# Kernel tuning notes

Measured on AMD Instinct MI355X. Metric: run time of the kernel, lower is better.

The kernel has to match this reference:

```python
import jax, jax.numpy as jnp
import numpy as np

HEADS = 4
AGENT = 49  # 7x7 agent tokens
LN_EPS = 1e-5


def setup_inputs() -> dict:
    key = jax.random.key(0)
    ks = jax.random.split(key, 3)
    B, C, H, W = 2, 128, 56, 56
    x = jax.random.normal(ks[0], (B, C, H, W), jnp.float32)
    # 1x1 convs == per-pixel linear maps; store as [out_ch, in_ch]
    w_qkv = jax.random.normal(ks[1], (3 * C, C), jnp.float32) * (C ** -0.5)
    w_proj = jax.random.normal(ks[2], (C, C), jnp.float32) * (C ** -0.5)
    b_proj = jnp.zeros((C,), jnp.float32)
    ln_g = jnp.ones((C,), jnp.float32)
    ln_b = jnp.zeros((C,), jnp.float32)
    return {"x": x, "w_qkv": w_qkv, "w_proj": w_proj, "b_proj": b_proj,
            "ln_g": ln_g, "ln_b": ln_b}


def reference(x, w_qkv, w_proj, b_proj, ln_g, ln_b):
    B, C, H, W = x.shape
    heads = HEADS
    hd = C // heads
    N = H * W
    scale = hd ** -0.5
    a = int(AGENT ** 0.5)  # 7; H,W divisible by a -> exact adaptive avg pool

    # 1x1-conv QKV: [B,3C,H,W] -> [B,3,heads,hd,N] -> q,k,v [B,h,N,hd]
    qkv = jnp.einsum('oc,bchw->bohw', w_qkv, x).reshape(B, 3, heads, hd, N)
    q = jnp.transpose(qkv[:, 0], (0, 1, 3, 2))
    k = jnp.transpose(qkv[:, 1], (0, 1, 3, 2))
    v = jnp.transpose(qkv[:, 2], (0, 1, 3, 2))

    # agent tokens: adaptive avg pool to (a,a) == uniform block mean
    agent = x.reshape(B, C, a, H // a, a, W // a).mean(axis=(3, 5))  # [B,C,a,a]
    agent = agent.reshape(B, heads, hd, AGENT)
    agent = jnp.transpose(agent, (0, 1, 3, 2))  # [B,h,A,hd]

    # stage 1: compress q through agent tokens
    q_to_agent = jax.nn.softmax(
        jnp.einsum('bhnd,bhad->bhna', q * scale, agent), axis=-1)  # [B,h,N,A]
    q_compressed = jnp.einsum('bhna,bhad->bhnd', q_to_agent, agent)  # [B,h,N,hd]

    # stage 2: full N x N attention with compressed queries
    attn = jax.nn.softmax(
        jnp.einsum('bhnd,bhmd->bhnm', q_compressed * scale, k), axis=-1)
    out = jnp.einsum('bhnm,bhmd->bhnd', attn, v)  # [B,h,N,hd]

    # merge heads -> [B,N,C], 1x1-conv proj, LayerNorm over C
    out = jnp.transpose(out, (0, 2, 1, 3)).reshape(B, N, C)
    out = jnp.einsum('bnc,oc->bno', out, w_proj) + b_proj
    mu = out.mean(-1, keepdims=True)
    var = out.var(-1, keepdims=True)
    out = (out - mu) / jnp.sqrt(var + LN_EPS) * ln_g + ln_b
    return jnp.transpose(out.reshape(B, H, W, C), (0, 3, 1, 2))
```

## Files before the change

### kernel.cpp

```cpp
#include <hip/hip_runtime.h>
#include <hip/hip_bf16.h>
#include <stdint.h>

typedef unsigned short u16;
typedef __attribute__((ext_vector_type(8))) short short8;
typedef __attribute__((ext_vector_type(4))) short short4v;
typedef __attribute__((ext_vector_type(4))) float f32x4;

#define NB 2
#define NC 128
#define NHD 4
#define HD 32
#define NN 3136
#define NA 49
#define NSPLIT 4
#define NKP 3200
#define NTILE 25
#define SCALE 0.17677669529663687f
#define LOG2E 1.4426950408889634f
#define QSC (SCALE * LOG2E)

__device__ inline u16 bfb(float f) {
    __hip_bfloat16 h = __float2bfloat16(f);
    return *(u16*)&h;
}
__device__ inline float b2f(u16 w) {
    return __uint_as_float(((uint32_t)w) << 16);
}
__device__ inline short4v pack4(float a, float b, float c, float d) {
    union { short4v s; __hip_bfloat162 h[2]; } u;
    u.h[0] = __float22bfloat162_rn(make_float2(a, b));
    u.h[1] = __float22bfloat162_rn(make_float2(c, d));
    return u.s;
}
__device__ inline float ldf(const void* p, size_t i, int f) {
    return f ? b2f(((const u16*)p)[i]) : ((const float*)p)[i];
}
__device__ inline void gld16(const u16* g, u16* l) {
    __builtin_amdgcn_global_load_lds(
        (__attribute__((address_space(1))) void*)(g),
        (__attribute__((address_space(3))) void*)(l), 16, 0, 0);
}
__device__ inline void stage8k(const u16* g, u16* lds, int w, int lane) {
    gld16(g + (size_t)(w * 64 + lane) * 8,       lds + (size_t)w * 512);
    gld16(g + (size_t)(256 + w * 64 + lane) * 8, lds + 2048 + (size_t)w * 512);
}
__device__ inline int detect_local(const u16* raw, int t) {
    __shared__ int cnt;
    if (t == 0) cnt = 0;
    __syncthreads();
    float a = fabsf(b2f(raw[t * 97]));
    if (a >= 1e-4f && a <= 100.0f) atomicAdd(&cnt, 1);
    __syncthreads();
    return cnt >= 230;
}

__global__ __launch_bounds__(256) void k_prep(const void* __restrict__ xr,
                                              const void* __restrict__ wq,
                                              const void* __restrict__ wp,
                                              const void* __restrict__ bp,
                                              const void* __restrict__ g,
                                              const void* __restrict__ bb,
                                              u16* __restrict__ xTs,
                                              u16* __restrict__ wbf,
                                              u16* __restrict__ wps,
                                              float* __restrict__ bgb,
                                              u16* __restrict__ agb,
                                              u16* __restrict__ agT,
                                              int* __restrict__ flagOut) {
    __shared__ u16 tile[128][18];
    int bx = blockIdx.x, t = threadIdx.x;
    int f = detect_local((const u16*)xr, t);
    if (bx < 392) {
        int b = bx / 196;
        int n0 = (bx % 196) * 16;
        int T = n0 >> 6, nbase = n0 & 63;
        int c = t >> 1, nh = (t & 1) * 8;
        size_t src = ((size_t)(b * 128 + c)) * NN + n0 + nh;
#pragma unroll
        for (int i = 0; i < 8; ++i) tile[c][nh + i] = bfb(ldf(xr, src + i, f));
        __syncthreads();
        int n = t >> 4, ktu = t & 15;
        int c0 = ktu * 8;
        short8 o;
#pragma unroll
        for (int i = 0; i < 8; ++i) o[i] = (short)tile[c0 + i][n];
        *(short8*)&xTs[(((size_t)b * 49 + T) * 16 + ktu) * 512 + (nbase + n) * 8] = o;
    } else if (bx < 584) {
        int i = (bx - 392) * 256 + t;
        wbf[i] = bfb(ldf(wq, i, f));
    } else if (bx < 648) {
        int i = (bx - 584) * 256 + t;
        int o = i >> 7, c = i & 127;
        int otile = o >> 4, oloc = o & 15, ktu = c >> 3, wi = c & 7;
        wps[((otile * 16 + ktu) * 16 + oloc) * 8 + wi] = bfb(ldf(wp, i, f));
    } else if (bx < 650) {
        int i = (bx - 648) * 256 + t;
        if (i < 128)      bgb[i] = ldf(bp, i, f);
        else if (i < 256) bgb[i] = ldf(g, i - 128, f);
        else if (i < 384) bgb[i] = ldf(bb, i - 256, f);
        if (bx == 648 && t == 0) *flagOut = f;
    } else {
        int idx = (bx - 650) * 256 + t;
        const int NPOOL = NB * NC * NA;
        if (idx < NPOOL) {
            int b = idx / (NC * NA);
            int r = idx % (NC * NA);
            int c = r / NA;
            int a = r % NA;
            int ai = a / 7, aj = a % 7;
            size_t base = ((size_t)(b * NC + c)) * NN + ai * 8 * 56 + aj * 8;
            float s = 0.f;
            if (f) {
                const u16* xp = (const u16*)xr + base;
#pragma unroll
                for (int uu = 0; uu < 8; ++uu) {
                    ushort4 a0 = *(const ushort4*)&xp[uu * 56];
                    ushort4 a1 = *(const ushort4*)&xp[uu * 56 + 4];
                    s += b2f(a0.x) + b2f(a0.y) + b2f(a0.z) + b2f(a0.w)
                       + b2f(a1.x) + b2f(a1.y) + b2f(a1.z) + b2f(a1.w);
                }
            } else {
                const float* xp = (const float*)xr + base;
#pragma unroll
                for (int uu = 0; uu < 8; ++uu) {
                    float4 v0 = *(const float4*)&xp[uu * 56];
                    float4 v1 = *(const float4*)&xp[uu * 56 + 4];
                    s += v0.x + v0.y + v0.z + v0.w + v1.x + v1.y + v1.z + v1.w;
                }
            }
            int h = c >> 5, d = c & 31;
            int bh = b * NHD + h;
            u16 val = bfb(s * (1.f / 64.f));
            agb[bh * 2048 + a * 32 + d] = val;
            agT[bh * 2048 + d * 64 + a] = val;
        } else {
            int j = idx - NPOOL;
            if (j < 3840) {
                int bh = j / 480, rem = j % 480;
                int a = 49 + rem / 32, d = rem % 32;
                agb[bh * 2048 + a * 32 + d] = 0;
            } else if (j < 7680) {
                j -= 3840;
                int bh = j / 480, rem = j % 480;
                int a = 49 + rem / 32, d = rem % 32;
                agT[bh * 2048 + d * 64 + a] = 0;
            }
        }
    }
}

__global__ __launch_bounds__(256, 4) void k_qkv_s1(const u16* __restrict__ xTs,
                                                   const u16* __restrict__ wbf,
                                                   const u16* __restrict__ agb,
                                                   const u16* __restrict__ agT,
                                                   u16* __restrict__ kbf,
                                                   u16* __restrict__ vtb,
                                                   u16* __restrict__ qcb) {
    __shared__ __align__(16) u16 xs[8192];
    __shared__ u16 qtile[2 * 64 * 40];
    int b = blockIdx.z;
    int n0 = blockIdx.x * 64;
    int w = threadIdx.x >> 6, lane = threadIdx.x & 63;
    int c = lane & 15, u = lane >> 4;
    int t = threadIdx.x;
    const u16* xtile = xTs + (((size_t)b * 49 + (n0 >> 6)) * 16) * 512;
#pragma unroll
    for (int i = 0; i < 4; ++i)
        gld16(xtile + (size_t)(i * 256 + t) * 8, xs + (size_t)(i * 256 + t) * 8);
    int o0 = blockIdx.y * 64 + w * 16;
    const f32x4 z = {0.f, 0.f, 0.f, 0.f};
    short8 af0 = *(const short8*)&wbf[(o0 + c) * 128 +  0 + u * 8];
    short8 af1 = *(const short8*)&wbf[(o0 + c) * 128 + 32 + u * 8];
    short8 af2 = *(const short8*)&wbf[(o0 + c) * 128 + 64 + u * 8];
    short8 af3 = *(const short8*)&wbf[(o0 + c) * 128 + 96 + u * 8];
    int tq = o0 >> 7, h = (o0 >> 5) & 3, d0 = (o0 & 31) + u * 4;
    size_t bh = (size_t)b * NHD + h;
    __syncthreads();
#pragma unroll
    for (int nt = 0; nt < 4; ++nt) {
        int n = n0 + nt * 16 + c;
        f32x4 acc = z;
        acc = __builtin_amdgcn_mfma_f32_16x16x32_bf16(af0,
            *(const short8*)&xs[((0 * 4 + u) * 64 + nt * 16 + c) * 8], acc, 0, 0, 0);
        acc = __builtin_amdgcn_mfma_f32_16x16x32_bf16(af1,
            *(const short8*)&xs[((1 * 4 + u) * 64 + nt * 16 + c) * 8], acc, 0, 0, 0);
        acc = __builtin_amdgcn_mfma_f32_16x16x32_bf16(af2,
            *(const short8*)&xs[((2 * 4 + u) * 64 + nt * 16 + c) * 8], acc, 0, 0, 0);
        acc = __builtin_amdgcn_mfma_f32_16x16x32_bf16(af3,
            *(const short8*)&xs[((3 * 4 + u) * 64 + nt * 16 + c) * 8], acc, 0, 0, 0);
        if (tq == 0) {
            int hl = (o0 >> 5) & 1;
            *(short4v*)&qtile[(hl * 64 + nt * 16 + c) * 40 + d0] =
                pack4(acc[0] * QSC, acc[1] * QSC, acc[2] * QSC, acc[3] * QSC);
        } else if (tq == 1) {
            int tile = n >> 7, sub = (n >> 4) & 7, key = n & 15;
            int dg = d0 >> 3, wi = d0 & 7;
            size_t kb0 = (((size_t)bh * NTILE + tile) * 8 + sub) * 4 + dg;
            *(short4v*)&kbf[kb0 * 128 + key * 8 + wi] =
                pack4(acc[0], acc[1], acc[2], acc[3]);
        } else {
            int tile = n >> 7, kt2 = n & 127;
            int sub = kt2 >> 4, uu = (kt2 >> 2) & 3, jj = n & 3;
            size_t vb0 = ((size_t)bh * NTILE + tile) * 4096 + sub * 512 + uu * 128 + jj;
#pragma unroll
            for (int r = 0; r < 4; ++r)
                vtb[vb0 + (d0 + r) * 4] = bfb(acc[r]);
        }
    }
    if (blockIdx.y < 2) {
        __syncthreads();
#pragma unroll
        for (int tt = w; tt < 8; tt += 4) {
            int hl2 = tt >> 2, r0 = (tt & 3) * 16;
            int hg = blockIdx.y * 2 + hl2;
            size_t bh2 = (size_t)b * NHD + hg;
            const u16* aB = agb + bh2 * 2048;
            const u16* aT = agT + bh2 * 2048;
            short8 qf = *(const short8*)&qtile[(hl2 * 64 + r0 + c) * 40 + u * 8];
            f32x4 st[4];
#pragma unroll
            for (int t2 = 0; t2 < 4; ++t2) {
                short8 afr = *(const short8*)&aB[(t2 * 16 + c) * 32 + u * 8];
                st[t2] = __builtin_amdgcn_mfma_f32_16x16x32_bf16(afr, qf, z, 0, 0, 0);
            }
            float e[4][4];
            float lsum = 0.f;
#pragma unroll
            for (int t2 = 0; t2 < 4; ++t2)
#pragma unroll
                for (int r = 0; r < 4; ++r) {
                    float v = __builtin_amdgcn_exp2f(st[t2][r]);
                    if (t2 == 3 && !(u == 0 && r == 0)) v = 0.f;
                    e[t2][r] = v;
                    lsum += v;
                }
            lsum += __shfl_xor(lsum, 16);
            lsum += __shfl_xor(lsum, 32);
            float linv = 1.f / lsum;
            f32x4 qlo = z, qhi = z;
#pragma unroll
            for (int t2 = 0; t2 < 4; ++t2) {
                short4v pf = pack4(e[t2][0] * linv, e[t2][1] * linv,
                                   e[t2][2] * linv, e[t2][3] * linv);
                short4v alo = *(const short4v*)&aT[c * 64 + t2 * 16 + u * 4];
                short4v ahi = *(const short4v*)&aT[(c + 16) * 64 + t2 * 16 + u * 4];
                qlo = __builtin_amdgcn_mfma_f32_16x16x16bf16_1k(alo, pf, qlo, 0, 0, 0);
                qhi = __builtin_amdgcn_mfma_f32_16x16x16bf16_1k(ahi, pf, qhi, 0, 0, 0);
            }
            u16* dst = &qcb[(bh2 * NN + n0 + r0 + c) * HD];
            *(short4v*)&dst[u * 4]      = pack4(qlo[0] * QSC, qlo[1] * QSC, qlo[2] * QSC, qlo[3] * QSC);
            *(short4v*)&dst[16 + u * 4] = pack4(qhi[0] * QSC, qhi[1] * QSC, qhi[2] * QSC, qhi[3] * QSC);
        }
    }
}

__global__ __launch_bounds__(256, 3) void k_flash4(const u16* __restrict__ qc,
                                                   const u16* __restrict__ kb,
                                                   const u16* __restrict__ vt,
                                                   u16* __restrict__ opb,
                                                   float* __restrict__ lp) {
    __shared__ __align__(16) u16 Ks[2][4096];
    __shared__ __align__(16) u16 Vs[2][4096];
    int b = blockIdx.z;
    int h = blockIdx.y & 3;
    int s = blockIdx.y >> 2;
    int w = threadIdx.x >> 6, lane = threadIdx.x & 63;
    int c = lane & 15, u = lane >> 4;
    int qa = blockIdx.x * 128 + w * 32;
    int qbr = qa + 16;
    if (qa  > NN - 16) qa  = NN - 16;
    if (qbr > NN - 16) qbr = NN - 16;
    size_t bh = (size_t)b * NHD + h;
    const u16* kg = kb + bh * (size_t)NTILE * 4096;
    const u16* vg = vt + bh * (size_t)NTILE * 4096;
    short8 qfA = *(const short8*)(qc + (bh * NN + qa  + c) * HD + u * 8);
    short8 qfB = *(const short8*)(qc + (bh * NN + qbr + c) * HD + u * 8);
    const f32x4 z = {0.f, 0.f, 0.f, 0.f};
    f32x4 oA0 = z, oA1 = z, oB0 = z, oB1 = z;
    float lA = 0.f, lB = 0.f;
    int t0 = (s * NTILE) / NSPLIT, t1 = ((s + 1) * NTILE) / NSPLIT;
    stage8k(kg + (size_t)t0 * 4096, &Ks[0][0], w, lane);
    stage8k(vg + (size_t)t0 * 4096, &Vs[0][0], w, lane);
#pragma unroll 1
    for (int t = t0; t < t1; ++t) {
        int buf = (t - t0) & 1;
        __syncthreads();
        if (t + 1 < t1) {
            stage8k(kg + (size_t)(t + 1) * 4096, &Ks[buf ^ 1][0], w, lane);
            stage8k(vg + (size_t)(t + 1) * 4096, &Vs[buf ^ 1][0], w, lane);
        }
        const u16* kp = &Ks[buf][0];
        const u16* vp = &Vs[buf][0];
        int kk = t * 128;
        bool tail = (kk + 128 > NN);
#pragma unroll
        for (int sub = 0; sub < 8; ++sub) {
            short8 kf = *(const short8*)(kp + ((sub * 4 + u) * 16 + c) * 8);
            f32x4 sA = __builtin_amdgcn_mfma_f32_16x16x32_bf16(kf, qfA, z, 0, 0, 0);
            f32x4 sB = __builtin_amdgcn_mfma_f32_16x16x32_bf16(kf, qfB, z, 0, 0, 0);
            float eA[4], eB[4];
#pragma unroll
            for (int r = 0; r < 4; ++r) {
                eA[r] = __builtin_amdgcn_exp2f(sA[r]);
                eB[r] = __builtin_amdgcn_exp2f(sB[r]);
            }
            if (tail) {
#pragma unroll
                for (int r = 0; r < 4; ++r)
                    if (kk + sub * 16 + u * 4 + r >= NN) { eA[r] = 0.f; eB[r] = 0.f; }
            }
            lA += (eA[0] + eA[1]) + (eA[2] + eA[3]);
            lB += (eB[0] + eB[1]) + (eB[2] + eB[3]);
            short4v pA = pack4(eA[0], eA[1], eA[2], eA[3]);
            short4v pB = pack4(eB[0], eB[1], eB[2], eB[3]);
            short4v va = *(const short4v*)(vp + sub * 512 + u * 128 + c * 4);
            short4v vb = *(const short4v*)(vp + sub * 512 + u * 128 + (c + 16) * 4);
            oA0 = __builtin_amdgcn_mfma_f32_16x16x16bf16_1k(va, pA, oA0, 0, 0, 0);
            oA1 = __builtin_amdgcn_mfma_f32_16x16x16bf16_1k(vb, pA, oA1, 0, 0, 0);
            oB0 = __builtin_amdgcn_mfma_f32_16x16x16bf16_1k(va, pB, oB0, 0, 0, 0);
            oB1 = __builtin_amdgcn_mfma_f32_16x16x16bf16_1k(vb, pB, oB1, 0, 0, 0);
        }
    }
    lA += __shfl_xor(lA, 16); lA += __shfl_xor(lA, 32);
    lB += __shfl_xor(lB, 16); lB += __shfl_xor(lB, 32);
    float iA = 1.f / lA, iB = 1.f / lB;
    u16* oba = opb + (((size_t)(s * NB + b)) * NN + qa + c) * NC + h * HD;
    *(short4v*)&oba[u * 4]      = pack4(oA0[0] * iA, oA0[1] * iA, oA0[2] * iA, oA0[3] * iA);
    *(short4v*)&oba[16 + u * 4] = pack4(oA1[0] * iA, oA1[1] * iA, oA1[2] * iA, oA1[3] * iA);
    u16* obb = opb + (((size_t)(s * NB + b)) * NN + qbr + c) * NC + h * HD;
    *(short4v*)&obb[u * 4]      = pack4(oB0[0] * iB, oB0[1] * iB, oB0[2] * iB, oB0[3] * iB);
    *(short4v*)&obb[16 + u * 4] = pack4(oB1[0] * iB, oB1[1] * iB, oB1[2] * iB, oB1[3] * iB);
    if (u == 0) {
        lp[(((size_t)(s * NB + b)) * NHD + h) * NN + qa  + c] = lA;
        lp[(((size_t)(s * NB + b)) * NHD + h) * NN + qbr + c] = lB;
    }
}

__global__ __launch_bounds__(256, 4) void k_proj2(const u16* __restrict__ opb,
                                                  const float* __restrict__ lp,
                                                  const u16* __restrict__ wps,
                                                  const float* __restrict__ bgb,
                                                  void* __restrict__ out,
                                                  const int* __restrict__ flag) {
    __shared__ __align__(16) u16 wl[16384];
    __shared__ u16 Af[16 * 136];
    __shared__ float red1[4][16], red2[4][16];
    int bx = blockIdx.x;
    int b = bx >= 196;
    int n0 = (bx - b * 196) * 16;
    int t = threadIdx.x;
#pragma unroll
    for (int i = 0; i < 8; ++i)
        gld16(wps + (size_t)(i * 256 + t) * 8, wl + (size_t)(i * 256 + t) * 8);
    {
        int row = t >> 4, c8 = (t & 15) * 8;
        int n = n0 + row;
        int hh = c8 >> 5;
        float num[8] = {};
        float den = 0.f;
#pragma unroll
        for (int s = 0; s < NSPLIT; ++s) {
            float ls = lp[(((size_t)(s * NB + b)) * NHD + hh) * NN + n];
            short8 o8 = *(const short8*)&opb[(((size_t)(s * NB + b)) * NN + n) * NC + c8];
            den += ls;
#pragma unroll
            for (int i = 0; i < 8; ++i) num[i] += ls * b2f((u16)o8[i]);
        }
        float inv = 1.f / den;
        u16* dst = &Af[row * 136 + c8];
#pragma unroll
        for (int i = 0; i < 8; i += 2) {
            __hip_bfloat162 p = __float22bfloat162_rn(
                make_float2(num[i] * inv, num[i + 1] * inv));
            *(uint32_t*)&dst[i] = *(uint32_t*)&p;
        }
    }
    __syncthreads();
    int w = t >> 6, lane = t & 63, c = lane & 15, u = lane >> 4;
    int oA = w * 32 + c, oB = w * 32 + 16 + c;
    const f32x4 z = {0.f, 0.f, 0.f, 0.f};
    f32x4 cA = z, cB = z;
#pragma unroll
    for (int kf = 0; kf < 4; ++kf) {
        short8 a  = *(const short8*)&Af[c * 136 + kf * 32 + u * 8];
        short8 bA = *(const short8*)&wl[(((2 * w) * 16 + kf * 4 + u) * 16 + c) * 8];
        short8 bB = *(const short8*)&wl[(((2 * w + 1) * 16 + kf * 4 + u) * 16 + c) * 8];
        cA = __builtin_amdgcn_mfma_f32_16x16x32_bf16(a, bA, cA, 0, 0, 0);
        cB = __builtin_amdgcn_mfma_f32_16x16x32_bf16(a, bB, cB, 0, 0, 0);
    }
    float bpA = bgb[oA], bpB = bgb[oB];
    float s1[4], s2[4];
#pragma unroll
    for (int r = 0; r < 4; ++r) {
        cA[r] += bpA; cB[r] += bpB;
        s1[r] = cA[r] + cB[r];
        s2[r] = cA[r] * cA[r] + cB[r] * cB[r];
    }
#pragma unroll
    for (int off = 1; off < 16; off <<= 1)
#pragma unroll
        for (int r = 0; r < 4; ++r) {
            s1[r] += __shfl_xor(s1[r], off);
            s2[r] += __shfl_xor(s2[r], off);
        }
    if (c == 0)
#pragma unroll
        for (int r = 0; r < 4; ++r) {
            red1[w][u * 4 + r] = s1[r];
            red2[w][u * 4 + r] = s2[r];
        }
    __syncthreads();
    float gA = bgb[128 + oA], beA = bgb[256 + oA];
    float gB = bgb[128 + oB], beB = bgb[256 + oB];
    float outA[4], outB[4];
#pragma unroll
    for (int r = 0; r < 4; ++r) {
        int row = u * 4 + r;
        float S1 = (red1[0][row] + red1[1][row]) + (red1[2][row] + red1[3][row]);
        float S2 = (red2[0][row] + red2[1][row]) + (red2[2][row] + red2[3][row]);
        float mu = S1 * (1.f / NC);
        float ex = S2 * (1.f / NC);
        float rstd = rsqrtf(ex - mu * mu + 1e-5f);
        outA[r] = (cA[r] - mu) * rstd * gA + beA;
        outB[r] = (cB[r] - mu) * rstd * gB + beB;
    }
    int n = n0 + u * 4;
    if (*flag) {
        __hip_bfloat16* ob = (__hip_bfloat16*)out;
        ushort4 sA = make_ushort4(bfb(outA[0]), bfb(outA[1]), bfb(outA[2]), bfb(outA[3]));
        ushort4 sB = make_ushort4(bfb(outB[0]), bfb(outB[1]), bfb(outB[2]), bfb(outB[3]));
        *(ushort4*)&ob[((size_t)(b * NC + oA)) * NN + n] = sA;
        *(ushort4*)&ob[((size_t)(b * NC + oB)) * NN + n] = sB;
    } else {
        float* ob = (float*)out;
        *(float4*)&ob[((size_t)(b * NC + oA)) * NN + n] = make_float4(outA[0], outA[1], outA[2], outA[3]);
        *(float4*)&ob[((size_t)(b * NC + oB)) * NN + n] = make_float4(outB[0], outB[1], outB[2], outB[3]);
    }
}

extern "C" void kernel_launch(void* const* d_in, const int* in_sizes, int n_in,
                              void* d_out, int out_size, void* d_ws, size_t ws_size,
                              hipStream_t stream) {
    const void* x_raw  = d_in[0];
    const void* wq_raw = d_in[1];
    const void* wp_raw = d_in[2];
    const void* bp_raw = d_in[3];
    const void* lg_raw = d_in[4];
    const void* lb_raw = d_in[5];

    float* ws   = (float*)d_ws;
    int*   flag = (int*)d_ws;
    float* bgb  = ws + 16;
    float* lp   = bgb + 512;
    u16*   opb  = (u16*)(lp + (size_t)NSPLIT * NB * NHD * NN);
    u16*   xTs  = opb + (size_t)NSPLIT * NB * NN * NC;
    u16*   wbf  = xTs + (size_t)NB * NN * NC;
    u16*   wps  = wbf + 3 * NC * NC;
    u16*   kbf  = wps + NC * NC;
    u16*   vtb  = kbf + (size_t)NB * NHD * NTILE * 4096;
    u16*   qcb  = vtb + (size_t)NB * NHD * NTILE * 4096;
    u16*   agb  = qcb + (size_t)NB * NHD * NN * HD;
    u16*   agT  = agb + NB * NHD * 64 * 32;

    k_prep<<<729, 256, 0, stream>>>(x_raw, wq_raw, wp_raw, bp_raw, lg_raw, lb_raw,
                                    xTs, wbf, wps, bgb, agb, agT, flag);
    k_qkv_s1<<<dim3(NN / 64, 6, NB), 256, 0, stream>>>(xTs, wbf, agb, agT,
                                                       kbf, vtb, qcb);
    k_flash4<<<dim3(25, NHD * NSPLIT, NB), 256, 0, stream>>>(qcb, kbf, vtb, opb, lp);
    k_proj2<<<392, 256, 0, stream>>>(opb, lp, wps, bgb, d_out, flag);
}
```

Measured before the change: 115.5 us.

## Fuse four kernels into one persistent kernel with software grid barriers

```diff
diff --git a/kernel.cpp b/kernel.cpp
--- a/kernel.cpp
+++ b/kernel.cpp
@@ -14,8 +14,8 @@
 #define NN 3136
 #define NA 49
 #define NSPLIT 4
-#define NKP 3200
 #define NTILE 25
+#define GRID 800
 #define SCALE 0.17677669529663687f
 #define LOG2E 1.4426950408889634f
 #define QSC (SCALE * LOG2E)
@@ -45,63 +45,72 @@
     gld16(g + (size_t)(w * 64 + lane) * 8,       lds + (size_t)w * 512);
     gld16(g + (size_t)(256 + w * 64 + lane) * 8, lds + 2048 + (size_t)w * 512);
 }
-__device__ inline int detect_local(const u16* raw, int t) {
-    __shared__ int cnt;
-    if (t == 0) cnt = 0;
+
+__device__ inline void gridbar(int* bar, int p) {
     __syncthreads();
-    float a = fabsf(b2f(raw[t * 97]));
-    if (a >= 1e-4f && a <= 100.0f) atomicAdd(&cnt, 1);
+    if (threadIdx.x == 0) {
+        __threadfence();
+        atomicAdd(&bar[p], 1);
+        while (__hip_atomic_load(&bar[p], __ATOMIC_RELAXED,
+                                 __HIP_MEMORY_SCOPE_AGENT) < GRID)
+            __builtin_amdgcn_s_sleep(2);
+        __threadfence();
+    }
     __syncthreads();
-    return cnt >= 230;
-}
-
-__global__ __launch_bounds__(256) void k_prep(const void* __restrict__ xr,
-                                              const void* __restrict__ wq,
-                                              const void* __restrict__ wp,
-                                              const void* __restrict__ bp,
-                                              const void* __restrict__ g,
-                                              const void* __restrict__ bb,
-                                              u16* __restrict__ xTs,
-                                              u16* __restrict__ wbf,
-                                              u16* __restrict__ wps,
-                                              float* __restrict__ bgb,
-                                              u16* __restrict__ agb,
-                                              u16* __restrict__ agT,
-                                              int* __restrict__ flagOut) {
-    __shared__ u16 tile[128][18];
-    int bx = blockIdx.x, t = threadIdx.x;
-    int f = detect_local((const u16*)xr, t);
-    if (bx < 392) {
-        int b = bx / 196;
-        int n0 = (bx % 196) * 16;
-        int T = n0 >> 6, nbase = n0 & 63;
-        int c = t >> 1, nh = (t & 1) * 8;
-        size_t src = ((size_t)(b * 128 + c)) * NN + n0 + nh;
-#pragma unroll
-        for (int i = 0; i < 8; ++i) tile[c][nh + i] = bfb(ldf(xr, src + i, f));
-        __syncthreads();
-        int n = t >> 4, ktu = t & 15;
-        int c0 = ktu * 8;
-        short8 o;
-#pragma unroll
-        for (int i = 0; i < 8; ++i) o[i] = (short)tile[c0 + i][n];
-        *(short8*)&xTs[(((size_t)b * 49 + T) * 16 + ktu) * 512 + (nbase + n) * 8] = o;
-    } else if (bx < 584) {
-        int i = (bx - 392) * 256 + t;
+}
+
+__global__ void k_init(int* __restrict__ bar) {
+    if (threadIdx.x < 8) bar[threadIdx.x] = 0;
+}
+
+__global__ __launch_bounds__(256, 4) void k_fused(const void* __restrict__ xr,
+                                                  const void* __restrict__ wq,
+                                                  const void* __restrict__ wp,
+                                                  const void* __restrict__ bp,
+                                                  const void* __restrict__ g,
+                                                  const void* __restrict__ bb,
+                                                  int* __restrict__ bar,
+                                                  float* __restrict__ bgb,
+                                                  float* __restrict__ lp,
+                                                  u16* __restrict__ opb,
+                                                  u16* __restrict__ wbf,
+                                                  u16* __restrict__ wps,
+                                                  u16* __restrict__ kbf,
+                                                  u16* __restrict__ vtb,
+                                                  u16* __restrict__ qcb,
+                                                  u16* __restrict__ agb,
+                                                  u16* __restrict__ agT,
+                                                  void* __restrict__ out) {
+    __shared__ __align__(16) u16 smem[18816];
+    __shared__ int dcnt;
+    int bid = blockIdx.x;
+    int t = threadIdx.x;
+    const f32x4 z = {0.f, 0.f, 0.f, 0.f};
+
+    if (t == 0) dcnt = 0;
+    __syncthreads();
+    {
+        float a = fabsf(b2f(((const u16*)xr)[t * 97]));
+        if (a >= 1e-4f && a <= 100.0f) atomicAdd(&dcnt, 1);
+    }
+    __syncthreads();
+    int f = (dcnt >= 230);
+
+    if (bid < 192) {
+        int i = bid * 256 + t;
         wbf[i] = bfb(ldf(wq, i, f));
-    } else if (bx < 648) {
-        int i = (bx - 584) * 256 + t;
+    } else if (bid < 256) {
+        int i = (bid - 192) * 256 + t;
         int o = i >> 7, c = i & 127;
-        int otile = o >> 4, oloc = o & 15, ktu = c >> 3, wi = c & 7;
-        wps[((otile * 16 + ktu) * 16 + oloc) * 8 + wi] = bfb(ldf(wp, i, f));
-    } else if (bx < 650) {
-        int i = (bx - 648) * 256 + t;
+        wps[(((o >> 4) * 16 + (c >> 3)) * 16 + (o & 15)) * 8 + (c & 7)] =
+            bfb(ldf(wp, i, f));
+    } else if (bid < 258) {
+        int i = (bid - 256) * 256 + t;
         if (i < 128)      bgb[i] = ldf(bp, i, f);
         else if (i < 256) bgb[i] = ldf(g, i - 128, f);
         else if (i < 384) bgb[i] = ldf(bb, i - 256, f);
-        if (bx == 648 && t == 0) *flagOut = f;
-    } else {
-        int idx = (bx - 650) * 256 + t;
+    } else if (bid < 337) {
+        int idx = (bid - 258) * 256 + t;
         const int NPOOL = NB * NC * NA;
         if (idx < NPOOL) {
             int b = idx / (NC * NA);
@@ -148,294 +157,314 @@
             }
         }
     }
-}
-
-__global__ __launch_bounds__(256, 4) void k_qkv_s1(const u16* __restrict__ xTs,
-                                                   const u16* __restrict__ wbf,
-                                                   const u16* __restrict__ agb,
-                                                   const u16* __restrict__ agT,
-                                                   u16* __restrict__ kbf,
-                                                   u16* __restrict__ vtb,
-                                                   u16* __restrict__ qcb) {
-    __shared__ __align__(16) u16 xs[8192];
-    __shared__ u16 qtile[2 * 64 * 40];
-    int b = blockIdx.z;
-    int n0 = blockIdx.x * 64;
-    int w = threadIdx.x >> 6, lane = threadIdx.x & 63;
-    int c = lane & 15, u = lane >> 4;
-    int t = threadIdx.x;
-    const u16* xtile = xTs + (((size_t)b * 49 + (n0 >> 6)) * 16) * 512;
-#pragma unroll
-    for (int i = 0; i < 4; ++i)
-        gld16(xtile + (size_t)(i * 256 + t) * 8, xs + (size_t)(i * 256 + t) * 8);
-    int o0 = blockIdx.y * 64 + w * 16;
-    const f32x4 z = {0.f, 0.f, 0.f, 0.f};
-    short8 af0 = *(const short8*)&wbf[(o0 + c) * 128 +  0 + u * 8];
-    short8 af1 = *(const short8*)&wbf[(o0 + c) * 128 + 32 + u * 8];
-    short8 af2 = *(const short8*)&wbf[(o0 + c) * 128 + 64 + u * 8];
-    short8 af3 = *(const short8*)&wbf[(o0 + c) * 128 + 96 + u * 8];
-    int tq = o0 >> 7, h = (o0 >> 5) & 3, d0 = (o0 & 31) + u * 4;
-    size_t bh = (size_t)b * NHD + h;
-    __syncthreads();
-#pragma unroll
-    for (int nt = 0; nt < 4; ++nt) {
-        int n = n0 + nt * 16 + c;
-        f32x4 acc = z;
-        acc = __builtin_amdgcn_mfma_f32_16x16x32_bf16(af0,
-            *(const short8*)&xs[((0 * 4 + u) * 64 + nt * 16 + c) * 8], acc, 0, 0, 0);
-        acc = __builtin_amdgcn_mfma_f32_16x16x32_bf16(af1,
-            *(const short8*)&xs[((1 * 4 + u) * 64 + nt * 16 + c) * 8], acc, 0, 0, 0);
-        acc = __builtin_amdgcn_mfma_f32_16x16x32_bf16(af2,
-            *(const short8*)&xs[((2 * 4 + u) * 64 + nt * 16 + c) * 8], acc, 0, 0, 0);
-        acc = __builtin_amdgcn_mfma_f32_16x16x32_bf16(af3,
-            *(const short8*)&xs[((3 * 4 + u) * 64 + nt * 16 + c) * 8], acc, 0, 0, 0);
-        if (tq == 0) {
-            int hl = (o0 >> 5) & 1;
-            *(short4v*)&qtile[(hl * 64 + nt * 16 + c) * 40 + d0] =
-                pack4(acc[0] * QSC, acc[1] * QSC, acc[2] * QSC, acc[3] * QSC);
-        } else if (tq == 1) {
-            int tile = n >> 7, sub = (n >> 4) & 7, key = n & 15;
-            int dg = d0 >> 3, wi = d0 & 7;
-            size_t kb0 = (((size_t)bh * NTILE + tile) * 8 + sub) * 4 + dg;
-            *(short4v*)&kbf[kb0 * 128 + key * 8 + wi] =
-                pack4(acc[0], acc[1], acc[2], acc[3]);
+    gridbar(bar, 0);
+
+    if (bid < 588) {
+        int B = bid / 294;
+        int r = bid % 294;
+        int y = r / 49;
+        int X = r % 49;
+        int n0 = X * 64;
+        u16* xs   = smem;
+        u16* tmp  = smem + 8192;
+        u16* qtile = smem + 8192;
+        {
+            int c = t >> 1, half = t & 1;
+            size_t base = ((size_t)(B * 128 + c)) * NN + n0 + half * 32;
+            u16 vals[32];
+            if (f) {
+                const u16* xp = (const u16*)xr + base;
+#pragma unroll
+                for (int j = 0; j < 4; ++j) {
+                    short8 v = *(const short8*)&xp[j * 8];
+#pragma unroll
+                    for (int e = 0; e < 8; ++e) vals[j * 8 + e] = (u16)v[e];
+                }
+            } else {
+                const float* xp = (const float*)xr + base;
+#pragma unroll
+                for (int j = 0; j < 8; ++j) {
+                    float4 v = *(const float4*)&xp[j * 4];
+                    vals[j * 4 + 0] = bfb(v.x); vals[j * 4 + 1] = bfb(v.y);
+                    vals[j * 4 + 2] = bfb(v.z); vals[j * 4 + 3] = bfb(v.w);
+                }
+            }
+#pragma unroll
+            for (int i = 0; i < 32; ++i)
+                tmp[c * 65 + half * 32 + i] = vals[i];
+        }
+        __syncthreads();
+#pragma unroll
+        for (int k = 0; k < 4; ++k) {
+            int j = k * 256 + t;
+            int gg = j >> 6, n = j & 63;
+            short8 o;
+#pragma unroll
+            for (int ci = 0; ci < 8; ++ci) o[ci] = (short)tmp[(gg * 8 + ci) * 65 + n];
+            *(short8*)&xs[(size_t)j * 8] = o;
+        }
+        int w = t >> 6, lane = t & 63;
+        int c = lane & 15, u = lane >> 4;
+        int o0 = y * 64 + w * 16;
+        short8 af0 = *(const short8*)&wbf[(o0 + c) * 128 +  0 + u * 8];
+        short8 af1 = *(const short8*)&wbf[(o0 + c) * 128 + 32 + u * 8];
+        short8 af2 = *(const short8*)&wbf[(o0 + c) * 128 + 64 + u * 8];
+        short8 af3 = *(const short8*)&wbf[(o0 + c) * 128 + 96 + u * 8];
+        int tq = o0 >> 7, h = (o0 >> 5) & 3, d0 = (o0 & 31) + u * 4;
+        size_t bh = (size_t)B * NHD + h;
+        __syncthreads();
+#pragma unroll
+        for (int nt = 0; nt < 4; ++nt) {
+            int n = n0 + nt * 16 + c;
+            f32x4 acc = z;
+            acc = __builtin_amdgcn_mfma_f32_16x16x32_bf16(af0,
+                *(const short8*)&xs[((0 * 4 + u) * 64 + nt * 16 + c) * 8], acc, 0, 0, 0);
+            acc = __builtin_amdgcn_mfma_f32_16x16x32_bf16(af1,
+                *(const short8*)&xs[((1 * 4 + u) * 64 + nt * 16 + c) * 8], acc, 0, 0, 0);
+            acc = __builtin_amdgcn_mfma_f32_16x16x32_bf16(af2,
+                *(const short8*)&xs[((2 * 4 + u) * 64 + nt * 16 + c) * 8], acc, 0, 0, 0);
+            acc = __builtin_amdgcn_mfma_f32_16x16x32_bf16(af3,
+                *(const short8*)&xs[((3 * 4 + u) * 64 + nt * 16 + c) * 8], acc, 0, 0, 0);
+            if (tq == 0) {
+                int hl = (o0 >> 5) & 1;
+                *(short4v*)&qtile[(hl * 64 + nt * 16 + c) * 40 + d0] =
+                    pack4(acc[0] * QSC, acc[1] * QSC, acc[2] * QSC, acc[3] * QSC);
+            } else if (tq == 1) {
+                int tile = n >> 7, sub = (n >> 4) & 7, key = n & 15;
+                int dg = d0 >> 3, wi = d0 & 7;
+                size_t kb0 = (((size_t)bh * NTILE + tile) * 8 + sub) * 4 + dg;
+                *(short4v*)&kbf[kb0 * 128 + key * 8 + wi] =
+                    pack4(acc[0], acc[1], acc[2], acc[3]);
+            } else {
+                int tile = n >> 7, kt2 = n & 127;
+                int sub = kt2 >> 4, uu = (kt2 >> 2) & 3, jj = n & 3;
+                size_t vb0 = ((size_t)bh * NTILE + tile) * 4096 + sub * 512 + uu * 128 + jj;
+#pragma unroll
+                for (int rr = 0; rr < 4; ++rr)
+                    vtb[vb0 + (d0 + rr) * 4] = bfb(acc[rr]);
+            }
+        }
+        if (y < 2) {
+            __syncthreads();
+#pragma unroll
+            for (int tt = w; tt < 8; tt += 4) {
+                int hl2 = tt >> 2, r0 = (tt & 3) * 16;
+                int hg = y * 2 + hl2;
+                size_t bh2 = (size_t)B * NHD + hg;
+                const u16* aB = agb + bh2 * 2048;
+                const u16* aT = agT + bh2 * 2048;
+                short8 qf = *(const short8*)&qtile[(hl2 * 64 + r0 + c) * 40 + u * 8];
+                f32x4 st[4];
+#pragma unroll
+                for (int t2 = 0; t2 < 4; ++t2) {
+                    short8 afr = *(const short8*)&aB[(t2 * 16 + c) * 32 + u * 8];
+                    st[t2] = __builtin_amdgcn_mfma_f32_16x16x32_bf16(afr, qf, z, 0, 0, 0);
+                }
+                float e[4][4];
+                float lsum = 0.f;
+#pragma unroll
+                for (int t2 = 0; t2 < 4; ++t2)
+#pragma unroll
+                    for (int rr = 0; rr < 4; ++rr) {
+                        float v = __builtin_amdgcn_exp2f(st[t2][rr]);
+                        if (t2 == 3 && !(u == 0 && rr == 0)) v = 0.f;
+                        e[t2][rr] = v;
+                        lsum += v;
+                    }
+                lsum += __shfl_xor(lsum, 16);
+                lsum += __shfl_xor(lsum, 32);
+                float linv = 1.f / lsum;
+                f32x4 qlo = z, qhi = z;
+#pragma unroll
+                for (int t2 = 0; t2 < 4; ++t2) {
+                    short4v pf = pack4(e[t2][0] * linv, e[t2][1] * linv,
+                                       e[t2][2] * linv, e[t2][3] * linv);
+                    short4v alo = *(const short4v*)&aT[c * 64 + t2 * 16 + u * 4];
+                    short4v ahi = *(const short4v*)&aT[(c + 16) * 64 + t2 * 16 + u * 4];
+                    qlo = __builtin_amdgcn_mfma_f32_16x16x16bf16_1k(alo, pf, qlo, 0, 0, 0);
+                    qhi = __builtin_amdgcn_mfma_f32_16x16x16bf16_1k(ahi, pf, qhi, 0, 0, 0);
+                }
+                u16* dst = &qcb[(bh2 * NN + n0 + r0 + c) * HD];
+                *(short4v*)&dst[u * 4]      = pack4(qlo[0] * QSC, qlo[1] * QSC, qlo[2] * QSC, qlo[3] * QSC);
+                *(short4v*)&dst[16 + u * 4] = pack4(qhi[0] * QSC, qhi[1] * QSC, qhi[2] * QSC, qhi[3] * QSC);
+            }
+        }
+    }
+    gridbar(bar, 1);
+
+    {
+        u16* KsB = smem;
+        u16* VsB = smem + 8192;
+        int qx = bid % 25;
+        int rem = bid / 25;
+        int h = rem & 3;
+        int s = (rem >> 2) & 3;
+        int B = rem >> 4;
+        int w = t >> 6, lane = t & 63;
+        int c = lane & 15, u = lane >> 4;
+        int qa = qx * 128 + w * 32;
+        int qbr = qa + 16;
+        if (qa  > NN - 16) qa  = NN - 16;
+        if (qbr > NN - 16) qbr = NN - 16;
+        size_t bh = (size_t)B * NHD + h;
+        const u16* kg = kbf + bh * (size_t)NTILE * 4096;
+        const u16* vg = vtb + bh * (size_t)NTILE * 4096;
+        short8 qfA = *(const short8*)(qcb + (bh * NN + qa  + c) * HD + u * 8);
+        short8 qfB = *(const short8*)(qcb + (bh * NN + qbr + c) * HD + u * 8);
+        f32x4 oA0 = z, oA1 = z, oB0 = z, oB1 = z;
+        float lA = 0.f, lB = 0.f;
+        int t0 = (s * NTILE) / NSPLIT, t1 = ((s + 1) * NTILE) / NSPLIT;
+        stage8k(kg + (size_t)t0 * 4096, KsB, w, lane);
+        stage8k(vg + (size_t)t0 * 4096, VsB, w, lane);
+#pragma unroll 1
+        for (int tt = t0; tt < t1; ++tt) {
+            int buf = (tt - t0) & 1;
+            __syncthreads();
+            if (tt + 1 < t1) {
+                stage8k(kg + (size_t)(tt + 1) * 4096, KsB + (buf ^ 1) * 4096, w, lane);
+                stage8k(vg + (size_t)(tt + 1) * 4096, VsB + (buf ^ 1) * 4096, w, lane);
+            }
+            const u16* kp = KsB + buf * 4096;
+            const u16* vp = VsB + buf * 4096;
+            int kk = tt * 128;
+            bool tail = (kk + 128 > NN);
+#pragma unroll
+            for (int sub = 0; sub < 8; ++sub) {
+                short8 kf = *(const short8*)(kp + ((sub * 4 + u) * 16 + c) * 8);
+                f32x4 sA = __builtin_amdgcn_mfma_f32_16x16x32_bf16(kf, qfA, z, 0, 0, 0);
+                f32x4 sB = __builtin_amdgcn_mfma_f32_16x16x32_bf16(kf, qfB, z, 0, 0, 0);
+                float eA[4], eB[4];
+#pragma unroll
+                for (int rr = 0; rr < 4; ++rr) {
+                    eA[rr] = __builtin_amdgcn_exp2f(sA[rr]);
+                    eB[rr] = __builtin_amdgcn_exp2f(sB[rr]);
+                }
+                if (tail) {
+#pragma unroll
+                    for (int rr = 0; rr < 4; ++rr)
+                        if (kk + sub * 16 + u * 4 + rr >= NN) { eA[rr] = 0.f; eB[rr] = 0.f; }
+                }
+                lA += (eA[0] + eA[1]) + (eA[2] + eA[3]);
+                lB += (eB[0] + eB[1]) + (eB[2] + eB[3]);
+                short4v pA = pack4(eA[0], eA[1], eA[2], eA[3]);
+                short4v pB = pack4(eB[0], eB[1], eB[2], eB[3]);
+                short4v va = *(const short4v*)(vp + sub * 512 + u * 128 + c * 4);
+                short4v vb = *(const short4v*)(vp + sub * 512 + u * 128 + (c + 16) * 4);
+                oA0 = __builtin_amdgcn_mfma_f32_16x16x16bf16_1k(va, pA, oA0, 0, 0, 0);
+                oA1 = __builtin_amdgcn_mfma_f32_16x16x16bf16_1k(vb, pA, oA1, 0, 0, 0);
+                oB0 = __builtin_amdgcn_mfma_f32_16x16x16bf16_1k(va, pB, oB0, 0, 0, 0);
+                oB1 = __builtin_amdgcn_mfma_f32_16x16x16bf16_1k(vb, pB, oB1, 0, 0, 0);
+            }
+        }
+        lA += __shfl_xor(lA, 16); lA += __shfl_xor(lA, 32);
+        lB += __shfl_xor(lB, 16); lB += __shfl_xor(lB, 32);
+        float iA = 1.f / lA, iB = 1.f / lB;
+        u16* oba = opb + (((size_t)(s * NB + B)) * NN + qa + c) * NC + h * HD;
+        *(short4v*)&oba[u * 4]      = pack4(oA0[0] * iA, oA0[1] * iA, oA0[2] * iA, oA0[3] * iA);
+        *(short4v*)&oba[16 + u * 4] = pack4(oA1[0] * iA, oA1[1] * iA, oA1[2] * iA, oA1[3] * iA);
+        u16* obb = opb + (((size_t)(s * NB + B)) * NN + qbr + c) * NC + h * HD;
+        *(short4v*)&obb[u * 4]      = pack4(oB0[0] * iB, oB0[1] * iB, oB0[2] * iB, oB0[3] * iB);
+        *(short4v*)&obb[16 + u * 4] = pack4(oB1[0] * iB, oB1[1] * iB, oB1[2] * iB, oB1[3] * iB);
+        if (u == 0) {
+            lp[(((size_t)(s * NB + B)) * NHD + h) * NN + qa  + c] = lA;
+            lp[(((size_t)(s * NB + B)) * NHD + h) * NN + qbr + c] = lB;
+        }
+    }
+    gridbar(bar, 2);
+
+    if (bid < 392) {
+        u16* wl = smem;
+        u16* Af = smem + 16384;
+        float* red1 = (float*)(smem + 18560);
+        float* red2 = red1 + 64;
+        int b = bid >= 196;
+        int n0 = (bid - b * 196) * 16;
+#pragma unroll
+        for (int i = 0; i < 8; ++i)
+            gld16(wps + (size_t)(i * 256 + t) * 8, wl + (size_t)(i * 256 + t) * 8);
+        {
+            int row = t >> 4, c8 = (t & 15) * 8;
+            int n = n0 + row;
+            int hh = c8 >> 5;
+            float num[8] = {};
+            float den = 0.f;
+#pragma unroll
+            for (int s = 0; s < NSPLIT; ++s) {
+                float ls = lp[(((size_t)(s * NB + b)) * NHD + hh) * NN + n];
+                short8 o8 = *(const short8*)&opb[(((size_t)(s * NB + b)) * NN + n) * NC + c8];
+                den += ls;
+#pragma unroll
+                for (int i = 0; i < 8; ++i) num[i] += ls * b2f((u16)o8[i]);
+            }
+            float inv = 1.f / den;
+            u16* dst = &Af[row * 136 + c8];
+#pragma unroll
+            for (int i = 0; i < 8; i += 2) {
+                __hip_bfloat162 p = __float22bfloat162_rn(
+                    make_float2(num[i] * inv, num[i + 1] * inv));
+                *(uint32_t*)&dst[i] = *(uint32_t*)&p;
+            }
+        }
+        __syncthreads();
+        int w = t >> 6, lane = t & 63, c = lane & 15, u = lane >> 4;
+        int oA = w * 32 + c, oB = w * 32 + 16 + c;
+        f32x4 cA = z, cB = z;
+#pragma unroll
+        for (int kf = 0; kf < 4; ++kf) {
+            short8 a  = *(const short8*)&Af[c * 136 + kf * 32 + u * 8];
+            short8 bA = *(const short8*)&wl[(((2 * w) * 16 + kf * 4 + u) * 16 + c) * 8];
+            short8 bB = *(const short8*)&wl[(((2 * w + 1) * 16 + kf * 4 + u) * 16 + c) * 8];
+            cA = __builtin_amdgcn_mfma_f32_16x16x32_bf16(a, bA, cA, 0, 0, 0);
+            cB = __builtin_amdgcn_mfma_f32_16x16x32_bf16(a, bB, cB, 0, 0, 0);
+        }
+        float bpA = bgb[oA], bpB = bgb[oB];
+        float s1[4], s2[4];
+#pragma unroll
+        for (int rr = 0; rr < 4; ++rr) {
+            cA[rr] += bpA; cB[rr] += bpB;
+            s1[rr] = cA[rr] + cB[rr];
+            s2[rr] = cA[rr] * cA[rr] + cB[rr] * cB[rr];
+        }
+#pragma unroll
+        for (int off = 1; off < 16; off <<= 1)
+#pragma unroll
+            for (int rr = 0; rr < 4; ++rr) {
+                s1[rr] += __shfl_xor(s1[rr], off);
+                s2[rr] += __shfl_xor(s2[rr], off);
+            }
+        if (c == 0)
+#pragma unroll
+            for (int rr = 0; rr < 4; ++rr) {
+                red1[w * 16 + u * 4 + rr] = s1[rr];
+                red2[w * 16 + u * 4 + rr] = s2[rr];
+            }
+        __syncthreads();
+        float gA = bgb[128 + oA], beA = bgb[256 + oA];
+        float gB = bgb[128 + oB], beB = bgb[256 + oB];
+        float outA[4], outB[4];
+#pragma unroll
+        for (int rr = 0; rr < 4; ++rr) {
+            int row = u * 4 + rr;
+            float S1 = (red1[0 * 16 + row] + red1[1 * 16 + row]) + (red1[2 * 16 + row] + red1[3 * 16 + row]);
+            float S2 = (red2[0 * 16 + row] + red2[1 * 16 + row]) + (red2[2 * 16 + row] + red2[3 * 16 + row]);
+            float mu = S1 * (1.f / NC);
+            float ex = S2 * (1.f / NC);
+            float rstd = rsqrtf(ex - mu * mu + 1e-5f);
+            outA[rr] = (cA[rr] - mu) * rstd * gA + beA;
+            outB[rr] = (cB[rr] - mu) * rstd * gB + beB;
+        }
+        int n = n0 + u * 4;
+        if (f) {
+            __hip_bfloat16* ob = (__hip_bfloat16*)out;
+            ushort4 sA = make_ushort4(bfb(outA[0]), bfb(outA[1]), bfb(outA[2]), bfb(outA[3]));
+            ushort4 sB = make_ushort4(bfb(outB[0]), bfb(outB[1]), bfb(outB[2]), bfb(outB[3]));
+            *(ushort4*)&ob[((size_t)(b * NC + oA)) * NN + n] = sA;
+            *(ushort4*)&ob[((size_t)(b * NC + oB)) * NN + n] = sB;
         } else {
-            int tile = n >> 7, kt2 = n & 127;
-            int sub = kt2 >> 4, uu = (kt2 >> 2) & 3, jj = n & 3;
-            size_t vb0 = ((size_t)bh * NTILE + tile) * 4096 + sub * 512 + uu * 128 + jj;
-#pragma unroll
-            for (int r = 0; r < 4; ++r)
-                vtb[vb0 + (d0 + r) * 4] = bfb(acc[r]);
-        }
-    }
-    if (blockIdx.y < 2) {
-        __syncthreads();
-#pragma unroll
-        for (int tt = w; tt < 8; tt += 4) {
-            int hl2 = tt >> 2, r0 = (tt & 3) * 16;
-            int hg = blockIdx.y * 2 + hl2;
-            size_t bh2 = (size_t)b * NHD + hg;
-            const u16* aB = agb + bh2 * 2048;
-            const u16* aT = agT + bh2 * 2048;
-            short8 qf = *(const short8*)&qtile[(hl2 * 64 + r0 + c) * 40 + u * 8];
-            f32x4 st[4];
-#pragma unroll
-            for (int t2 = 0; t2 < 4; ++t2) {
-                short8 afr = *(const short8*)&aB[(t2 * 16 + c) * 32 + u * 8];
-                st[t2] = __builtin_amdgcn_mfma_f32_16x16x32_bf16(afr, qf, z, 0, 0, 0);
-            }
-            float e[4][4];
-            float lsum = 0.f;
-#pragma unroll
-            for (int t2 = 0; t2 < 4; ++t2)
-#pragma unroll
-                for (int r = 0; r < 4; ++r) {
-                    float v = __builtin_amdgcn_exp2f(st[t2][r]);
-                    if (t2 == 3 && !(u == 0 && r == 0)) v = 0.f;
-                    e[t2][r] = v;
-                    lsum += v;
-                }
-            lsum += __shfl_xor(lsum, 16);
-            lsum += __shfl_xor(lsum, 32);
-            float linv = 1.f / lsum;
-            f32x4 qlo = z, qhi = z;
-#pragma unroll
-            for (int t2 = 0; t2 < 4; ++t2) {
-                short4v pf = pack4(e[t2][0] * linv, e[t2][1] * linv,
-                                   e[t2][2] * linv, e[t2][3] * linv);
-                short4v alo = *(const short4v*)&aT[c * 64 + t2 * 16 + u * 4];
-                short4v ahi = *(const short4v*)&aT[(c + 16) * 64 + t2 * 16 + u * 4];
-                qlo = __builtin_amdgcn_mfma_f32_16x16x16bf16_1k(alo, pf, qlo, 0, 0, 0);
-                qhi = __builtin_amdgcn_mfma_f32_16x16x16bf16_1k(ahi, pf, qhi, 0, 0, 0);
-            }
-            u16* dst = &qcb[(bh2 * NN + n0 + r0 + c) * HD];
-            *(short4v*)&dst[u * 4]      = pack4(qlo[0] * QSC, qlo[1] * QSC, qlo[2] * QSC, qlo[3] * QSC);
-            *(short4v*)&dst[16 + u * 4] = pack4(qhi[0] * QSC, qhi[1] * QSC, qhi[2] * QSC, qhi[3] * QSC);
-        }
-    }
-}
-
-__global__ __launch_bounds__(256, 3) void k_flash4(const u16* __restrict__ qc,
-                                                   const u16* __restrict__ kb,
-                                                   const u16* __restrict__ vt,
-                                                   u16* __restrict__ opb,
-                                                   float* __restrict__ lp) {
-    __shared__ __align__(16) u16 Ks[2][4096];
-    __shared__ __align__(16) u16 Vs[2][4096];
-    int b = blockIdx.z;
-    int h = blockIdx.y & 3;
-    int s = blockIdx.y >> 2;
-    int w = threadIdx.x >> 6, lane = threadIdx.x & 63;
-    int c = lane & 15, u = lane >> 4;
-    int qa = blockIdx.x * 128 + w * 32;
-    int qbr = qa + 16;
-    if (qa  > NN - 16) qa  = NN - 16;
-    if (qbr > NN - 16) qbr = NN - 16;
-    size_t bh = (size_t)b * NHD + h;
-    const u16* kg = kb + bh * (size_t)NTILE * 4096;
-    const u16* vg = vt + bh * (size_t)NTILE * 4096;
-    short8 qfA = *(const short8*)(qc + (bh * NN + qa  + c) * HD + u * 8);
-    short8 qfB = *(const short8*)(qc + (bh * NN + qbr + c) * HD + u * 8);
-    const f32x4 z = {0.f, 0.f, 0.f, 0.f};
-    f32x4 oA0 = z, oA1 = z, oB0 = z, oB1 = z;
-    float lA = 0.f, lB = 0.f;
-    int t0 = (s * NTILE) / NSPLIT, t1 = ((s + 1) * NTILE) / NSPLIT;
-    stage8k(kg + (size_t)t0 * 4096, &Ks[0][0], w, lane);
-    stage8k(vg + (size_t)t0 * 4096, &Vs[0][0], w, lane);
-#pragma unroll 1
-    for (int t = t0; t < t1; ++t) {
-        int buf = (t - t0) & 1;
-        __syncthreads();
-        if (t + 1 < t1) {
-            stage8k(kg + (size_t)(t + 1) * 4096, &Ks[buf ^ 1][0], w, lane);
-            stage8k(vg + (size_t)(t + 1) * 4096, &Vs[buf ^ 1][0], w, lane);
-        }
-        const u16* kp = &Ks[buf][0];
-        const u16* vp = &Vs[buf][0];
-        int kk = t * 128;
-        bool tail = (kk + 128 > NN);
-#pragma unroll
-        for (int sub = 0; sub < 8; ++sub) {
-            short8 kf = *(const short8*)(kp + ((sub * 4 + u) * 16 + c) * 8);
-            f32x4 sA = __builtin_amdgcn_mfma_f32_16x16x32_bf16(kf, qfA, z, 0, 0, 0);
-            f32x4 sB = __builtin_amdgcn_mfma_f32_16x16x32_bf16(kf, qfB, z, 0, 0, 0);
-            float eA[4], eB[4];
-#pragma unroll
-            for (int r = 0; r < 4; ++r) {
-                eA[r] = __builtin_amdgcn_exp2f(sA[r]);
-                eB[r] = __builtin_amdgcn_exp2f(sB[r]);
-            }
-            if (tail) {
-#pragma unroll
-                for (int r = 0; r < 4; ++r)
-                    if (kk + sub * 16 + u * 4 + r >= NN) { eA[r] = 0.f; eB[r] = 0.f; }
-            }
-            lA += (eA[0] + eA[1]) + (eA[2] + eA[3]);
-            lB += (eB[0] + eB[1]) + (eB[2] + eB[3]);
-            short4v pA = pack4(eA[0], eA[1], eA[2], eA[3]);
-            short4v pB = pack4(eB[0], eB[1], eB[2], eB[3]);
-            short4v va = *(const short4v*)(vp + sub * 512 + u * 128 + c * 4);
-            short4v vb = *(const short4v*)(vp + sub * 512 + u * 128 + (c + 16) * 4);
-            oA0 = __builtin_amdgcn_mfma_f32_16x16x16bf16_1k(va, pA, oA0, 0, 0, 0);
-            oA1 = __builtin_amdgcn_mfma_f32_16x16x16bf16_1k(vb, pA, oA1, 0, 0, 0);
-            oB0 = __builtin_amdgcn_mfma_f32_16x16x16bf16_1k(va, pB, oB0, 0, 0, 0);
-            oB1 = __builtin_amdgcn_mfma_f32_16x16x16bf16_1k(vb, pB, oB1, 0, 0, 0);
-        }
-    }
-    lA += __shfl_xor(lA, 16); lA += __shfl_xor(lA, 32);
-    lB += __shfl_xor(lB, 16); lB += __shfl_xor(lB, 32);
-    float iA = 1.f / lA, iB = 1.f / lB;
-    u16* oba = opb + (((size_t)(s * NB + b)) * NN + qa + c) * NC + h * HD;
-    *(short4v*)&oba[u * 4]      = pack4(oA0[0] * iA, oA0[1] * iA, oA0[2] * iA, oA0[3] * iA);
-    *(short4v*)&oba[16 + u * 4] = pack4(oA1[0] * iA, oA1[1] * iA, oA1[2] * iA, oA1[3] * iA);
-    u16* obb = opb + (((size_t)(s * NB + b)) * NN + qbr + c) * NC + h * HD;
-    *(short4v*)&obb[u * 4]      = pack4(oB0[0] * iB, oB0[1] * iB, oB0[2] * iB, oB0[3] * iB);
-    *(short4v*)&obb[16 + u * 4] = pack4(oB1[0] * iB, oB1[1] * iB, oB1[2] * iB, oB1[3] * iB);
-    if (u == 0) {
-        lp[(((size_t)(s * NB + b)) * NHD + h) * NN + qa  + c] = lA;
-        lp[(((size_t)(s * NB + b)) * NHD + h) * NN + qbr + c] = lB;
-    }
-}
-
-__global__ __launch_bounds__(256, 4) void k_proj2(const u16* __restrict__ opb,
-                                                  const float* __restrict__ lp,
-                                                  const u16* __restrict__ wps,
-                                                  const float* __restrict__ bgb,
-                                                  void* __restrict__ out,
-                                                  const int* __restrict__ flag) {
-    __shared__ __align__(16) u16 wl[16384];
-    __shared__ u16 Af[16 * 136];
-    __shared__ float red1[4][16], red2[4][16];
-    int bx = blockIdx.x;
-    int b = bx >= 196;
-    int n0 = (bx - b * 196) * 16;
-    int t = threadIdx.x;
-#pragma unroll
-    for (int i = 0; i < 8; ++i)
-        gld16(wps + (size_t)(i * 256 + t) * 8, wl + (size_t)(i * 256 + t) * 8);
-    {
-        int row = t >> 4, c8 = (t & 15) * 8;
-        int n = n0 + row;
-        int hh = c8 >> 5;
-        float num[8] = {};
-        float den = 0.f;
-#pragma unroll
-        for (int s = 0; s < NSPLIT; ++s) {
-            float ls = lp[(((size_t)(s * NB + b)) * NHD + hh) * NN + n];
-            short8 o8 = *(const short8*)&opb[(((size_t)(s * NB + b)) * NN + n) * NC + c8];
-            den += ls;
-#pragma unroll
-            for (int i = 0; i < 8; ++i) num[i] += ls * b2f((u16)o8[i]);
-        }
-        float inv = 1.f / den;
-        u16* dst = &Af[row * 136 + c8];
-#pragma unroll
-        for (int i = 0; i < 8; i += 2) {
-            __hip_bfloat162 p = __float22bfloat162_rn(
-                make_float2(num[i] * inv, num[i + 1] * inv));
-            *(uint32_t*)&dst[i] = *(uint32_t*)&p;
-        }
-    }
-    __syncthreads();
-    int w = t >> 6, lane = t & 63, c = lane & 15, u = lane >> 4;
-    int oA = w * 32 + c, oB = w * 32 + 16 + c;
-    const f32x4 z = {0.f, 0.f, 0.f, 0.f};
-    f32x4 cA = z, cB = z;
-#pragma unroll
-    for (int kf = 0; kf < 4; ++kf) {
-        short8 a  = *(const short8*)&Af[c * 136 + kf * 32 + u * 8];
-        short8 bA = *(const short8*)&wl[(((2 * w) * 16 + kf * 4 + u) * 16 + c) * 8];
-        short8 bB = *(const short8*)&wl[(((2 * w + 1) * 16 + kf * 4 + u) * 16 + c) * 8];
-        cA = __builtin_amdgcn_mfma_f32_16x16x32_bf16(a, bA, cA, 0, 0, 0);
-        cB = __builtin_amdgcn_mfma_f32_16x16x32_bf16(a, bB, cB, 0, 0, 0);
-    }
-    float bpA = bgb[oA], bpB = bgb[oB];
-    float s1[4], s2[4];
-#pragma unroll
-    for (int r = 0; r < 4; ++r) {
-        cA[r] += bpA; cB[r] += bpB;
-        s1[r] = cA[r] + cB[r];
-        s2[r] = cA[r] * cA[r] + cB[r] * cB[r];
-    }
-#pragma unroll
-    for (int off = 1; off < 16; off <<= 1)
-#pragma unroll
-        for (int r = 0; r < 4; ++r) {
-            s1[r] += __shfl_xor(s1[r], off);
-            s2[r] += __shfl_xor(s2[r], off);
-        }
-    if (c == 0)
-#pragma unroll
-        for (int r = 0; r < 4; ++r) {
-            red1[w][u * 4 + r] = s1[r];
-            red2[w][u * 4 + r] = s2[r];
-        }
-    __syncthreads();
-    float gA = bgb[128 + oA], beA = bgb[256 + oA];
-    float gB = bgb[128 + oB], beB = bgb[256 + oB];
-    float outA[4], outB[4];
-#pragma unroll
-    for (int r = 0; r < 4; ++r) {
-        int row = u * 4 + r;
-        float S1 = (red1[0][row] + red1[1][row]) + (red1[2][row] + red1[3][row]);
-        float S2 = (red2[0][row] + red2[1][row]) + (red2[2][row] + red2[3][row]);
-        float mu = S1 * (1.f / NC);
-        float ex = S2 * (1.f / NC);
-        float rstd = rsqrtf(ex - mu * mu + 1e-5f);
-        outA[r] = (cA[r] - mu) * rstd * gA + beA;
-        outB[r] = (cB[r] - mu) * rstd * gB + beB;
-    }
-    int n = n0 + u * 4;
-    if (*flag) {
-        __hip_bfloat16* ob = (__hip_bfloat16*)out;
-        ushort4 sA = make_ushort4(bfb(outA[0]), bfb(outA[1]), bfb(outA[2]), bfb(outA[3]));
-        ushort4 sB = make_ushort4(bfb(outB[0]), bfb(outB[1]), bfb(outB[2]), bfb(outB[3]));
-        *(ushort4*)&ob[((size_t)(b * NC + oA)) * NN + n] = sA;
-        *(ushort4*)&ob[((size_t)(b * NC + oB)) * NN + n] = sB;
-    } else {
-        float* ob = (float*)out;
-        *(float4*)&ob[((size_t)(b * NC + oA)) * NN + n] = make_float4(outA[0], outA[1], outA[2], outA[3]);
-        *(float4*)&ob[((size_t)(b * NC + oB)) * NN + n] = make_float4(outB[0], outB[1], outB[2], outB[3]);
+            float* ob = (float*)out;
+            *(float4*)&ob[((size_t)(b * NC + oA)) * NN + n] = make_float4(outA[0], outA[1], outA[2], outA[3]);
+            *(float4*)&ob[((size_t)(b * NC + oB)) * NN + n] = make_float4(outB[0], outB[1], outB[2], outB[3]);
+        }
     }
 }
 
@@ -449,13 +478,11 @@
     const void* lg_raw = d_in[4];
     const void* lb_raw = d_in[5];
 
-    float* ws   = (float*)d_ws;
-    int*   flag = (int*)d_ws;
-    float* bgb  = ws + 16;
+    int*   bar  = (int*)d_ws;
+    float* bgb  = (float*)d_ws + 16;
     float* lp   = bgb + 512;
     u16*   opb  = (u16*)(lp + (size_t)NSPLIT * NB * NHD * NN);
-    u16*   xTs  = opb + (size_t)NSPLIT * NB * NN * NC;
-    u16*   wbf  = xTs + (size_t)NB * NN * NC;
+    u16*   wbf  = opb + (size_t)NSPLIT * NB * NN * NC;
     u16*   wps  = wbf + 3 * NC * NC;
     u16*   kbf  = wps + NC * NC;
     u16*   vtb  = kbf + (size_t)NB * NHD * NTILE * 4096;
@@ -463,10 +490,8 @@
     u16*   agb  = qcb + (size_t)NB * NHD * NN * HD;
     u16*   agT  = agb + NB * NHD * 64 * 32;
 
-    k_prep<<<729, 256, 0, stream>>>(x_raw, wq_raw, wp_raw, bp_raw, lg_raw, lb_raw,
-                                    xTs, wbf, wps, bgb, agb, agT, flag);
-    k_qkv_s1<<<dim3(NN / 64, 6, NB), 256, 0, stream>>>(xTs, wbf, agb, agT,
-                                                       kbf, vtb, qcb);
-    k_flash4<<<dim3(25, NHD * NSPLIT, NB), 256, 0, stream>>>(qcb, kbf, vtb, opb, lp);
-    k_proj2<<<392, 256, 0, stream>>>(opb, lp, wps, bgb, d_out, flag);
-}
+    k_init<<<1, 64, 0, stream>>>(bar);
+    k_fused<<<GRID, 256, 0, stream>>>(x_raw, wq_raw, wp_raw, bp_raw, lg_raw,
+                                      lb_raw, bar, bgb, lp, opb, wbf, wps,
+                                      kbf, vtb, qcb, agb, agT, d_out);
+}
```

New measurement: 385.0 us. +233.3%, slower.
